# Performance work log

Hardware: AMD Instinct MI355X
Metric: run time of the kernel (lower is better)

## Reference

```python
import jax, jax.numpy as jnp
import numpy as np

B, CIN, H, W = 2, 32, 64, 64
COUT, K, PAD = 32, 3, 1
KK = K * K
PRED_W = COUT * CIN * KK  # 9216 dynamic-weight channels
PRED_OUT = PRED_W + COUT  # + per-pixel bias
EPS = 1e-12


def setup_inputs() -> dict:
    key = jax.random.key(0)
    k1, k2 = jax.random.split(key)
    x = jax.random.normal(k1, (B, CIN, H, W), dtype=jnp.float32)
    # 1x1-conv predictor weights (Conv2d(in_ch, pred_out, 1)), fan-in scaled
    Wp = jax.random.normal(k2, (PRED_OUT, CIN), dtype=jnp.float32) / np.sqrt(CIN).astype(np.float32)
    bp = jnp.zeros((PRED_OUT,), dtype=jnp.float32)
    return {"x": x, "Wp": Wp, "bp": bp}


def _unfold3x3(x):
    # F.unfold with k=3, pad=1, stride=1, dilation=1 -> (B, Cin, 9, L), c slowest then (kh, kw)
    xp = jnp.pad(x, ((0, 0), (0, 0), (PAD, PAD), (PAD, PAD)))
    patches = jnp.stack(
        [xp[:, :, i:i + H, j:j + W] for i in range(K) for j in range(K)], axis=2
    )  # (B, Cin, 9, H, W)
    return patches.reshape(B, CIN, KK, H * W)


def _l2norm(v, axis):
    n = jnp.sqrt(jnp.sum(v * v, axis=axis, keepdims=True))
    return v / jnp.maximum(n, EPS)


def reference(x, Wp, bp):
    L = H * W
    patches = _unfold3x3(x)  # (B, Cin, 9, L)
    # 1x1 conv predictor (stride=1 path -> operates on x directly)
    pred = jnp.einsum('oc,bchw->bohw', Wp, x) + bp[None, :, None, None]  # (B, PRED_OUT, H, W)
    dyn_w = pred[:, :PRED_W].reshape(B, COUT, CIN, KK, L)
    dyn_b = pred[:, PRED_W:].reshape(B, COUT, L)
    # norm_pred: L2-normalize over Cin axis, then over k*k axis
    dyn_w = _l2norm(dyn_w, axis=2)
    dyn_w = _l2norm(dyn_w, axis=3)
    out = jnp.einsum('bockl,bckl->bol', dyn_w, patches) + dyn_b  # (B, Cout, L)
    return out.reshape(B, COUT, H, W)
```

## Files before the change

kernel.cpp:

```cpp
#include <hip/hip_runtime.h>

#define TPB 256
#define WQ_BYTES 589824

typedef __attribute__((ext_vector_type(8))) short short8;
typedef __attribute__((ext_vector_type(4))) float f32x4;

__device__ __forceinline__ unsigned f2bf_pk(float a, float b) {
  return ((__float_as_uint(a) + 0x8000u) >> 16) | ((__float_as_uint(b) + 0x8000u) & 0xffff0000u);
}
__device__ __forceinline__ float bflo(unsigned v) { return __uint_as_float(v << 16); }
__device__ __forceinline__ float bfhi(unsigned v) { return __uint_as_float(v & 0xffff0000u); }

__device__ __forceinline__ float swap16_add(float v) {
  auto r = __builtin_amdgcn_permlane16_swap(__float_as_uint(v), __float_as_uint(v), false, false);
  return __uint_as_float(r[0]) + __uint_as_float(r[1]);
}
__device__ __forceinline__ float swap32_add(float v) {
  auto r = __builtin_amdgcn_permlane32_swap(__float_as_uint(v), __float_as_uint(v), false, false);
  return __uint_as_float(r[0]) + __uint_as_float(r[1]);
}

__global__ void prep_kernel(const float* __restrict__ Wp, unsigned* __restrict__ Wq) {
  int idx = blockIdx.x * blockDim.x + threadIdx.x;
  if (idx >= 32 * 18 * 64 * 4) return;
  int j2   = idx & 3;
  int lane = (idx >> 2) & 63;
  int rt   = (idx >> 8) % 18;
  int o    = (idx >> 8) / 18;
  int m16 = lane & 15, kq = lane >> 4;
  int row = o * 288 + (m16 >> 2) * 72 + rt * 4 + (m16 & 3);
  const float* src = Wp + row * 32 + kq * 8 + j2 * 2;
  Wq[idx] = f2bf_pk(src[0], src[1]);
}

template <bool USE_WQ>
__global__ __launch_bounds__(TPB, 4) void dppc9_kernel(
    const float* __restrict__ x, const float* __restrict__ Wp,
    const float* __restrict__ bp, const unsigned* __restrict__ Wq,
    float* __restrict__ out) {
  __shared__ __align__(16) unsigned short xrow2[3 * 66 * 40];
  __shared__ __align__(16) float bp_s[4 * 288];
  __shared__ __align__(16) float Wb_s[4 * 32];
  __shared__ float bias4[4];

  const int tid = threadIdx.x;
  const int bid = blockIdx.x;
  const int og  = bid & 7;
  const int t   = bid >> 3;
  const int b   = t >> 6;
  const int h   = t & 63;

  const char* wq_g = (const char*)Wq + (size_t)(og * 4) * 18432;

  for (int i = tid; i < 120; i += TPB) {
    int p = i / 20, w = i % 20;
    ((unsigned*)xrow2)[(((p >> 1) * 66 + ((p & 1) ? 65 : 0)) * 20) + w] = 0;
  }
  for (int i = tid; i < 1536; i += TPB) {
    int px_ = i & 63, c4 = (i >> 6) & 7, r = i >> 9;
    int hh = h - 1 + r;
    unsigned w0 = 0, w1 = 0;
    if ((unsigned)hh < 64u) {
      const float* xp = x + ((b * 32 + c4 * 4) * 64 + hh) * 64 + px_;
      float f0 = xp[0], f1 = xp[4096], f2 = xp[8192], f3 = xp[12288];
      w0 = f2bf_pk(f0, f1);
      w1 = f2bf_pk(f2, f3);
    }
    uint2* dst = (uint2*)&xrow2[(r * 66 + 1 + px_) * 40 + c4 * 4];
    *dst = make_uint2(w0, w1);
  }
  for (int i = tid; i < 1152; i += TPB) bp_s[i] = bp[og * 1152 + i];
  if (tid < 128) Wb_s[tid] = Wp[(9216 + og * 4 + (tid >> 5)) * 32 + (tid & 31)];
  if (tid < 4) bias4[tid] = bp[9216 + og * 4 + tid];
  __syncthreads();

  const int lane = tid & 63;
  const int wv   = tid >> 6;
  const int m16  = lane & 15, kq = lane >> 4;
  const int px   = wv * 16 + m16;

#pragma unroll 1
  for (int oo = 0; oo < 4; ++oo) {
    const int o = og * 4 + oo;

    const uint4 cent = *(const uint4*)&xrow2[(66 + 1 + px) * 40 + kq * 8];
    const short8 bfrag = *(const short8*)&cent;

    f32x4 acc[18];
    if (USE_WQ) {
      const char* ap = wq_g + ((oo * 1152 + lane) << 4);
      const float* bbp = &bp_s[oo * 288 + kq * 72];
      short8 aA[6], aB[6];
#pragma unroll
      for (int j = 0; j < 6; ++j) aA[j] = *(const short8*)(ap + (j << 10));
      __builtin_amdgcn_sched_barrier(0);
#pragma unroll
      for (int j = 0; j < 6; ++j) aB[j] = *(const short8*)(ap + ((6 + j) << 10));
      __builtin_amdgcn_sched_barrier(0);
#pragma unroll
      for (int j = 0; j < 6; ++j) {
        const f32x4 bb = *(const f32x4*)(bbp + j * 4);
        acc[j] = __builtin_amdgcn_mfma_f32_16x16x32_bf16(aA[j], bfrag, bb, 0, 0, 0);
      }
      __builtin_amdgcn_sched_barrier(0);
#pragma unroll
      for (int j = 0; j < 6; ++j) aA[j] = *(const short8*)(ap + ((12 + j) << 10));
      __builtin_amdgcn_sched_barrier(0);
#pragma unroll
      for (int j = 0; j < 6; ++j) {
        const f32x4 bb = *(const f32x4*)(bbp + (6 + j) * 4);
        acc[6 + j] = __builtin_amdgcn_mfma_f32_16x16x32_bf16(aB[j], bfrag, bb, 0, 0, 0);
      }
      __builtin_amdgcn_sched_barrier(0);
#pragma unroll
      for (int j = 0; j < 6; ++j) {
        const f32x4 bb = *(const f32x4*)(bbp + (12 + j) * 4);
        acc[12 + j] = __builtin_amdgcn_mfma_f32_16x16x32_bf16(aA[j], bfrag, bb, 0, 0, 0);
      }
      __builtin_amdgcn_sched_barrier(0);
    } else {
      const float* ab = Wp + (o * 288 + (m16 >> 2) * 72 + (m16 & 3)) * 32 + kq * 8;
#pragma unroll
      for (int rt = 0; rt < 18; ++rt) {
        const float* ap = ab + rt * 4 * 32;
        float4 a0 = *(const float4*)ap;
        float4 a1 = *(const float4*)(ap + 4);
        union { short8 v; unsigned u[4]; } af;
        af.u[0] = f2bf_pk(a0.x, a0.y);
        af.u[1] = f2bf_pk(a0.z, a0.w);
        af.u[2] = f2bf_pk(a1.x, a1.y);
        af.u[3] = f2bf_pk(a1.z, a1.w);
        const f32x4 bb = *(const f32x4*)&bp_s[oo * 288 + kq * 72 + rt * 4];
        acc[rt] = __builtin_amdgcn_mfma_f32_16x16x32_bf16(af.v, bfrag, bb, 0, 0, 0);
      }
    }

    float rinv[9];
#pragma unroll
    for (int kk = 0; kk < 9; ++kk) rinv[kk] = 0.f;
#pragma unroll
    for (int c8 = 0; c8 < 8; ++c8)
#pragma unroll
      for (int kk = 0; kk < 9; ++kk) {
        const int idx = c8 * 9 + kk;
        const float v = acc[idx >> 2][idx & 3];
        rinv[kk] += v * v;
      }
#pragma unroll
    for (int kk = 0; kk < 9; ++kk) {
      float s = rinv[kk];
      s = swap16_add(s);
      s = swap32_add(s);
      rinv[kk] = rsqrtf(fmaxf(s, 1e-24f));
    }

    float s2[8], dot[8];
#pragma unroll
    for (int c8 = 0; c8 < 8; ++c8) { s2[c8] = 0.f; dot[c8] = 0.f; }
#pragma unroll
    for (int kk = 0; kk < 9; ++kk) {
      const int kh = kk / 3, kw = kk - kh * 3;
      const uint4 tp = (kk == 4) ? cent
                                 : *(const uint4*)&xrow2[(kh * 66 + kw + px) * 40 + kq * 8];
      const float rv = rinv[kk];
#pragma unroll
      for (int c8 = 0; c8 < 8; ++c8) {
        const int idx = c8 * 9 + kk;
        const float tv = acc[idx >> 2][idx & 3] * rv;
        s2[c8] += tv * tv;
        const unsigned wd = ((const unsigned*)&tp)[c8 >> 1];
        const float pv = (c8 & 1) ? bfhi(wd) : bflo(wd);
        dot[c8] += tv * pv;
      }
    }

    const f32x4 wb0 = *(const f32x4*)&Wb_s[oo * 32 + kq * 8];
    const f32x4 wb1 = *(const f32x4*)&Wb_s[oo * 32 + kq * 8 + 4];
    float oacc = 0.f;
#pragma unroll
    for (int c8 = 0; c8 < 8; ++c8) {
      oacc += rsqrtf(fmaxf(s2[c8], 1e-24f)) * dot[c8];
      const unsigned wd = ((const unsigned*)&cent)[c8 >> 1];
      const float xc = (c8 & 1) ? bfhi(wd) : bflo(wd);
      const float wbv = (c8 < 4) ? wb0[c8] : wb1[c8 - 4];
      oacc += wbv * xc;
    }
    oacc = swap16_add(oacc);
    oacc = swap32_add(oacc);
    if (kq == 0)
      out[((b * 32 + o) * 64 + h) * 64 + px] = oacc + bias4[oo];
  }
}

extern "C" void kernel_launch(void* const* d_in, const int* in_sizes, int n_in,
                              void* d_out, int out_size, void* d_ws, size_t ws_size,
                              hipStream_t stream) {
  const float* x  = (const float*)d_in[0];
  const float* Wp = (const float*)d_in[1];
  const float* bp = (const float*)d_in[2];
  float* out = (float*)d_out;
  if (ws_size >= WQ_BYTES) {
    prep_kernel<<<576, 256, 0, stream>>>(Wp, (unsigned*)d_ws);
    dppc9_kernel<true><<<1024, TPB, 0, stream>>>(x, Wp, bp, (const unsigned*)d_ws, out);
  } else {
    dppc9_kernel<false><<<1024, TPB, 0, stream>>>(x, Wp, bp, nullptr, out);
  }
}
```

Before: 80.01 us.

## Stage bf16 predictor weights in LDS per block, drop separate prep kernel

New measurement: 85.85 us. 7.3% more time.

```diff
diff --git a/kernel.cpp b/kernel.cpp
--- a/kernel.cpp
+++ b/kernel.cpp
@@ -1,7 +1,6 @@
 #include <hip/hip_runtime.h>
 
 #define TPB 256
-#define WQ_BYTES 589824
 
 typedef __attribute__((ext_vector_type(8))) short short8;
 typedef __attribute__((ext_vector_type(4))) float f32x4;
@@ -21,25 +20,11 @@
   return __uint_as_float(r[0]) + __uint_as_float(r[1]);
 }
 
-__global__ void prep_kernel(const float* __restrict__ Wp, unsigned* __restrict__ Wq) {
-  int idx = blockIdx.x * blockDim.x + threadIdx.x;
-  if (idx >= 32 * 18 * 64 * 4) return;
-  int j2   = idx & 3;
-  int lane = (idx >> 2) & 63;
-  int rt   = (idx >> 8) % 18;
-  int o    = (idx >> 8) / 18;
-  int m16 = lane & 15, kq = lane >> 4;
-  int row = o * 288 + (m16 >> 2) * 72 + rt * 4 + (m16 & 3);
-  const float* src = Wp + row * 32 + kq * 8 + j2 * 2;
-  Wq[idx] = f2bf_pk(src[0], src[1]);
-}
-
-template <bool USE_WQ>
 __global__ __launch_bounds__(TPB, 4) void dppc9_kernel(
     const float* __restrict__ x, const float* __restrict__ Wp,
-    const float* __restrict__ bp, const unsigned* __restrict__ Wq,
-    float* __restrict__ out) {
+    const float* __restrict__ bp, float* __restrict__ out) {
   __shared__ __align__(16) unsigned short xrow2[3 * 66 * 40];
+  __shared__ __align__(16) char wqls[18432];
   __shared__ __align__(16) float bp_s[4 * 288];
   __shared__ __align__(16) float Wb_s[4 * 32];
   __shared__ float bias4[4];
@@ -51,7 +36,20 @@
   const int b   = t >> 6;
   const int h   = t & 63;
 
-  const char* wq_g = (const char*)Wq + (size_t)(og * 4) * 18432;
+
+#define STAGE_WQ(O_)                                                        \
+  do {                                                                      \
+    const int obase_ = (O_) * 9216;                                         \
+    for (int i = tid; i < 2304; i += TPB) {                                 \
+      const int e_ = i >> 1, hf_ = i & 1;                                   \
+      const int rt_ = e_ >> 6, lane_ = e_ & 63;                             \
+      const int m16_ = lane_ & 15, kq_ = lane_ >> 4;                        \
+      const int row_ = (m16_ >> 2) * 72 + rt_ * 4 + (m16_ & 3);             \
+      const float4 f_ = *(const float4*)(Wp + obase_ + row_ * 32 + kq_ * 8 + hf_ * 4); \
+      *(uint2*)(wqls + (e_ << 4) + (hf_ << 3)) =                            \
+          make_uint2(f2bf_pk(f_.x, f_.y), f2bf_pk(f_.z, f_.w));             \
+    }                                                                       \
+  } while (0)
 
   for (int i = tid; i < 120; i += TPB) {
     int p = i / 20, w = i % 20;
@@ -73,6 +71,7 @@
   for (int i = tid; i < 1152; i += TPB) bp_s[i] = bp[og * 1152 + i];
   if (tid < 128) Wb_s[tid] = Wp[(9216 + og * 4 + (tid >> 5)) * 32 + (tid & 31)];
   if (tid < 4) bias4[tid] = bp[9216 + og * 4 + tid];
+  STAGE_WQ(og * 4);
   __syncthreads();
 
   const int lane = tid & 63;
@@ -88,52 +87,11 @@
     const short8 bfrag = *(const short8*)&cent;
 
     f32x4 acc[18];
-    if (USE_WQ) {
-      const char* ap = wq_g + ((oo * 1152 + lane) << 4);
-      const float* bbp = &bp_s[oo * 288 + kq * 72];
-      short8 aA[6], aB[6];
 #pragma unroll
-      for (int j = 0; j < 6; ++j) aA[j] = *(const short8*)(ap + (j << 10));
-      __builtin_amdgcn_sched_barrier(0);
-#pragma unroll
-      for (int j = 0; j < 6; ++j) aB[j] = *(const short8*)(ap + ((6 + j) << 10));
-      __builtin_amdgcn_sched_barrier(0);
-#pragma unroll
-      for (int j = 0; j < 6; ++j) {
-        const f32x4 bb = *(const f32x4*)(bbp + j * 4);
-        acc[j] = __builtin_amdgcn_mfma_f32_16x16x32_bf16(aA[j], bfrag, bb, 0, 0, 0);
-      }
-      __builtin_amdgcn_sched_barrier(0);
-#pragma unroll
-      for (int j = 0; j < 6; ++j) aA[j] = *(const short8*)(ap + ((12 + j) << 10));
-      __builtin_amdgcn_sched_barrier(0);
-#pragma unroll
-      for (int j = 0; j < 6; ++j) {
-        const f32x4 bb = *(const f32x4*)(bbp + (6 + j) * 4);
-        acc[6 + j] = __builtin_amdgcn_mfma_f32_16x16x32_bf16(aB[j], bfrag, bb, 0, 0, 0);
-      }
-      __builtin_amdgcn_sched_barrier(0);
-#pragma unroll
-      for (int j = 0; j < 6; ++j) {
-        const f32x4 bb = *(const f32x4*)(bbp + (12 + j) * 4);
-        acc[12 + j] = __builtin_amdgcn_mfma_f32_16x16x32_bf16(aA[j], bfrag, bb, 0, 0, 0);
-      }
-      __builtin_amdgcn_sched_barrier(0);
-    } else {
-      const float* ab = Wp + (o * 288 + (m16 >> 2) * 72 + (m16 & 3)) * 32 + kq * 8;
-#pragma unroll
-      for (int rt = 0; rt < 18; ++rt) {
-        const float* ap = ab + rt * 4 * 32;
-        float4 a0 = *(const float4*)ap;
-        float4 a1 = *(const float4*)(ap + 4);
-        union { short8 v; unsigned u[4]; } af;
-        af.u[0] = f2bf_pk(a0.x, a0.y);
-        af.u[1] = f2bf_pk(a0.z, a0.w);
-        af.u[2] = f2bf_pk(a1.x, a1.y);
-        af.u[3] = f2bf_pk(a1.z, a1.w);
-        const f32x4 bb = *(const f32x4*)&bp_s[oo * 288 + kq * 72 + rt * 4];
-        acc[rt] = __builtin_amdgcn_mfma_f32_16x16x32_bf16(af.v, bfrag, bb, 0, 0, 0);
-      }
+    for (int rt = 0; rt < 18; ++rt) {
+      const short8 a = *(const short8*)(wqls + (rt * 64 + lane) * 16);
+      const f32x4 bb = *(const f32x4*)&bp_s[oo * 288 + kq * 72 + rt * 4];
+      acc[rt] = __builtin_amdgcn_mfma_f32_16x16x32_bf16(a, bfrag, bb, 0, 0, 0);
     }
 
     float rinv[9];
@@ -190,7 +148,14 @@
     oacc = swap32_add(oacc);
     if (kq == 0)
       out[((b * 32 + o) * 64 + h) * 64 + px] = oacc + bias4[oo];
+
+    if (oo < 3) {
+      __syncthreads();
+      STAGE_WQ(o + 1);
+      __syncthreads();
+    }
   }
+#undef STAGE_WQ
 }
 
 extern "C" void kernel_launch(void* const* d_in, const int* in_sizes, int n_in,
@@ -200,10 +165,6 @@
   const float* Wp = (const float*)d_in[1];
   const float* bp = (const float*)d_in[2];
   float* out = (float*)d_out;
-  if (ws_size >= WQ_BYTES) {
-    prep_kernel<<<576, 256, 0, stream>>>(Wp, (unsigned*)d_ws);
-    dppc9_kernel<true><<<1024, TPB, 0, stream>>>(x, Wp, bp, (const unsigned*)d_ws, out);
-  } else {
-    dppc9_kernel<false><<<1024, TPB, 0, stream>>>(x, Wp, bp, nullptr, out);
-  }
+  (void)d_ws; (void)ws_size;
+  dppc9_kernel<<<1024, TPB, 0, stream>>>(x, Wp, bp, out);
 }
```
